# Optimization experiments

Measured on AMD Instinct MI355X. Metric: run time of the kernel, lower is better.

## Reference

```python
import jax, jax.numpy as jnp
import numpy as np

TWO_PI = 2.0 * np.pi
D_IN, N, P, C, BATCH = 784, 1024, 128, 10, 256
T, BETA, K_COUP, A_ANC = 0.5, 2.0, 1.0, 0.08
OMEGA_ANC = TWO_PI * 200.0
N_STEPS = 16  # fixed-grid RK4 steps over [0, T]


def setup_inputs() -> dict:
    key = jax.random.key(0)
    k0, k1, k2, k3 = jax.random.split(key, 4)
    x = jax.random.normal(k0, (BATCH, D_IN), dtype=jnp.float32)
    W_enc = jax.random.normal(k1, (N, D_IN), dtype=jnp.float32) * (1.0 / np.sqrt(D_IN))
    b_enc = jnp.zeros((N,), dtype=jnp.float32)
    xi = jax.random.uniform(k2, (P, N), dtype=jnp.float32) * TWO_PI  # memory patterns
    W_out = jax.random.normal(k3, (C, 2 * N), dtype=jnp.float32) * (1.0 / np.sqrt(2 * N))
    b_out = jnp.zeros((C,), dtype=jnp.float32)
    return {"x": x, "W_enc": W_enc, "b_enc": b_enc, "xi": xi, "W_out": W_out, "b_out": b_out}


def _dphi(t, phi, xi):
    # phi: (B, N), xi: (P, N) -> diff: (B, P, N)
    diff = phi[:, None, :] - xi[None, :, :]
    m = jnp.cos(diff).sum(-1)                               # (B, P) overlaps
    w = jax.nn.softmax(BETA * m / N, axis=-1)               # (B, P)
    coupling = jnp.einsum('bp,bpn->bn', w, jnp.sin(diff))   # (B, N)
    return K_COUP * coupling + A_ANC * jnp.sin(OMEGA_ANC * t - phi)


def reference(x, W_enc, b_enc, xi, W_out, b_out):
    # Encoder: phi0 in (0, 2pi)
    phi0 = TWO_PI * jax.nn.sigmoid(x @ W_enc.T + b_enc)
    dt = T / N_STEPS

    def step(phi, t):
        k1 = _dphi(t, phi, xi)
        k2 = _dphi(t + 0.5 * dt, phi + 0.5 * dt * k1, xi)
        k3 = _dphi(t + 0.5 * dt, phi + 0.5 * dt * k2, xi)
        k4 = _dphi(t + dt, phi + dt * k3, xi)
        return phi + (dt / 6.0) * (k1 + 2.0 * k2 + 2.0 * k3 + k4), None

    ts = jnp.arange(N_STEPS, dtype=jnp.float32) * dt
    phi_T, _ = jax.lax.scan(step, phi0, ts)
    # Readout on [cos, sin] features
    feats = jnp.concatenate([jnp.cos(phi_T), jnp.sin(phi_T)], axis=-1)
    return feats @ W_out.T + b_out
```

## Files before the change

### kernel.cpp

```cpp
#include <hip/hip_runtime.h>
#include <math.h>


typedef __attribute__((ext_vector_type(4))) float f32x4;
typedef __attribute__((ext_vector_type(2))) float f32x2;
typedef __attribute__((ext_vector_type(8))) short bf16x8;
typedef __attribute__((ext_vector_type(2))) unsigned short u16x2;
typedef __attribute__((ext_vector_type(2))) long i64x2;

struct TCons { float s[64]; float c[64]; };

__device__ __forceinline__ unsigned short f2bf(float f) {
  unsigned u = __builtin_bit_cast(unsigned, f);
  return (unsigned short)((u + 0x7FFFu + ((u >> 16) & 1u)) >> 16);
}
__device__ __forceinline__ long pk8fp8(const float* v) {
  unsigned lo = __builtin_amdgcn_cvt_pk_fp8_f32(v[0], v[1], 0, false);
  lo = __builtin_amdgcn_cvt_pk_fp8_f32(v[2], v[3], lo, true);
  unsigned hi = __builtin_amdgcn_cvt_pk_fp8_f32(v[4], v[5], 0, false);
  hi = __builtin_amdgcn_cvt_pk_fp8_f32(v[6], v[7], hi, true);
  return (long)lo | ((long)hi << 32);
}

#define A1_OFF    0
#define MBUF_OFF  8192
#define W_OFF     10304
#define ZP_OFF    10560
#define XST_OFF   10576
#define T2L_OFF   13904
#define RED_OFF   13904
#define LDS_BYTES 161360

__global__
__attribute__((amdgpu_flat_work_group_size(1024, 1024), amdgpu_waves_per_eu(4, 4)))
void phasenn_kernel(
    const float* __restrict__ x, const float* __restrict__ W_enc,
    const float* __restrict__ b_enc, const float* __restrict__ xi,
    const float* __restrict__ W_out, const float* __restrict__ b_out,
    float* __restrict__ dout, char* __restrict__ wsb, TCons tc)
{
  __shared__ __align__(16) char smem[LDS_BYTES];

  const int tid  = threadIdx.x;
  const int bk   = blockIdx.x;
  const int w    = tid >> 6;
  const int lane = tid & 63;
  const int q    = lane >> 4;
  const int b16  = lane & 15;
  const int row2 = b16 & 1;
  const int j4   = b16 >> 2;
  const int rp   = (b16 >> 1) & 1;
  const int swz  = row2 * 5;

  char* T1g = wsb;
  char* T2g = wsb + (256 << 10);

  if (tid < 4) *(unsigned*)(smem + ZP_OFF + tid*4) = 0;

  {
    const int row = tid >> 7, dg = tid & 127;
    if (row < 2 && dg < 100) {
      bf16x8 fr = {0,0,0,0,0,0,0,0};
      if (dg < 98) {
        f32x4 v0 = *(const f32x4*)(x + (bk*2 + row)*784 + dg*8);
        f32x4 v1 = *(const f32x4*)(x + (bk*2 + row)*784 + dg*8 + 4);
        #pragma unroll
        for (int i = 0; i < 8; ++i) fr[i] = (short)f2bf(i < 4 ? v0[i] : v1[i-4]);
      }
      *(bf16x8*)(smem + XST_OFF + row*1664 + (((dg ^ row) & 127) << 4)) = fr;
    }
  }

  if (w < 8) {
    const int p = w*16 + b16;
    for (int f = 0; f < 32; ++f) {
      const int n0 = f*32 + q*8;
      f32x4 v0 = *(const f32x4*)(xi + p*1024 + n0);
      f32x4 v1 = *(const f32x4*)(xi + p*1024 + n0 + 4);
      float cv[8], sv[8];
      #pragma unroll
      for (int i = 0; i < 8; ++i) {
        float xv = (i < 4) ? v0[i] : v1[i-4];
        sv[i] = __sinf(xv); cv[i] = __cosf(xv);
      }
      i64x2 pr; pr[0] = pk8fp8(cv); pr[1] = pk8fp8(sv);
      *(i64x2*)(T1g + (size_t)((w*32 + f)*64 + lane)*16) = pr;
    }
  } else {
    const int w2 = w - 8;
    for (int f = 0; f < 32; ++f) {
      const int ct = w2*8 + (f >> 2), pt2 = f & 3;
      const int n = ct*16 + b16;
      float cv[8], sv[8];
      #pragma unroll
      for (int i = 0; i < 8; ++i) {
        float xv = xi[(pt2*32 + q*8 + i)*1024 + n];
        sv[i] = __sinf(xv); cv[i] = __cosf(xv);
      }
      i64x2 pr; pr[0] = pk8fp8(cv); pr[1] = pk8fp8(sv);
      if (ct < 36)
        *(i64x2*)(smem + T2L_OFF + (size_t)((ct*4 + pt2)*64 + lane)*16) = pr;
      else
        *(i64x2*)(T2g + (size_t)((ct*4 + pt2)*64 + lane)*16) = pr;
    }
  }
  __syncthreads();

  float p0[2], ka[2], pwv[2];
  {
    f32x4 pac[4] = {{0,0,0,0},{0,0,0,0},{0,0,0,0},{0,0,0,0}};
    for (int kt = 0; kt < 25; ++kt) {
      const char* baddr =
          smem + XST_OFF + row2*1664 + ((((kt*4 + q) ^ row2) & 127) << 4);
      bf16x8 bfr = *(const bf16x8*)baddr;
      const int d = kt*32 + q*8;
      #pragma unroll
      for (int j = 0; j < 4; ++j) {
        bf16x8 afr = {0,0,0,0,0,0,0,0};
        if (d < 784) {
          const int n = (w*4 + j)*16 + b16;
          f32x4 v0 = *(const f32x4*)(W_enc + n*784 + d);
          f32x4 v1 = *(const f32x4*)(W_enc + n*784 + d + 4);
          #pragma unroll
          for (int i = 0; i < 8; ++i) afr[i] = (short)f2bf(i < 4 ? v0[i] : v1[i-4]);
        }
        pac[j] = __builtin_amdgcn_mfma_f32_16x16x32_bf16(afr, bfr, pac[j], 0, 0, 0);
      }
    }
    f32x4 pc = (j4==0) ? pac[0] : (j4==1) ? pac[1] : (j4==2) ? pac[2] : pac[3];
    float vA = rp ? pc[2] : pc[0];
    float vB = rp ? pc[3] : pc[1];
    const int n0 = (w*4 + j4)*16 + q*4 + rp*2;
    float ph0 = 6.283185307179586f / (1.0f + __expf(-(vA + b_enc[n0])));
    float ph1 = 6.283185307179586f / (1.0f + __expf(-(vB + b_enc[n0 + 1])));
    p0[0] = ph0; pwv[0] = ph0; ka[0] = 0.0f;
    p0[1] = ph1; pwv[1] = ph1; ka[1] = 0.0f;
  }

  const float dtf = 0.03125f, half = 0.015625f;
  const float sixth = (float)(0.03125/6.0);

  for (int e = 0; e < 64; ++e) {
    float csv[2], snv[2];
    {
      #pragma unroll
      for (int r = 0; r < 2; ++r) {
        snv[r] = __sinf(pwv[r]);
        csv[r] = __cosf(pwv[r]);
      }
      unsigned cp = __builtin_amdgcn_cvt_pk_fp8_f32(csv[0], csv[1], 0, false);
      unsigned sp = __builtin_amdgcn_cvt_pk_fp8_f32(snv[0], snv[1], 0, false);
      const int u = (w*4 + j4)*2 + (q >> 1);
      char* base = smem + A1_OFF + row2*2048 + ((q & 1) << 2) + rp*2;
      *(unsigned short*)(base + ((u ^ swz) << 3))        = (unsigned short)cp;
      *(unsigned short*)(base + 1024 + ((u ^ swz) << 3)) = (unsigned short)sp;
    }
    __syncthreads();

    {
      const int pt = w & 7, kh = w >> 3;
      f32x4 accC = {0.f, 0.f, 0.f, 0.f}, accS = {0.f, 0.f, 0.f, 0.f};
      const char* t1b = T1g + (size_t)((pt*32 + kh*16)*64 + lane)*16;
      const char* a1b = smem + A1_OFF + row2*2048;
      #pragma unroll 8
      for (int i2 = 0; i2 < 16; ++i2) {
        const int ktc = kh*16 + i2;
        i64x2 af = *(const i64x2*)(t1b + (size_t)i2*1024);
        long bc = *(const long*)(a1b + (((ktc*4 + q) ^ swz) << 3));
        long bs = *(const long*)(a1b + 1024 + (((ktc*4 + q) ^ swz) << 3));
        accC = __builtin_amdgcn_mfma_f32_16x16x32_fp8_fp8(af[0], bc, accC, 0, 0, 0);
        accS = __builtin_amdgcn_mfma_f32_16x16x32_fp8_fp8(af[1], bs, accS, 0, 0, 0);
      }
      if (b16 < 2) {
        f32x4 acc = accC + accS;
        *(f32x4*)(smem + MBUF_OFF + kh*1056 + b16*528 + ((pt*16 + q*4) << 2)) = acc;
      }
    }
    __syncthreads();

    if (w < 2) {
      const char* mb = smem + MBUF_OFF + w*528 + lane*8;
      f32x2 u0 = *(const f32x2*)(mb);
      f32x2 u1 = *(const f32x2*)(mb + 1056);
      float e0 = __expf((u0[0] + u1[0]) * 0.001953125f);
      float e1 = __expf((u0[1] + u1[1]) * 0.001953125f);
      float s = e0 + e1;
      #pragma unroll
      for (int off = 1; off < 64; off <<= 1) s += __shfl_xor(s, off, 64);
      const float inv64 = 64.0f / s;
      unsigned pk = __builtin_amdgcn_cvt_pk_fp8_f32(e0*inv64, e1*inv64, 0, false);
      const int pp = lane*2, u = pp >> 3;
      *(unsigned short*)(smem + W_OFF + w*128 + ((u ^ w) << 3) + (pp & 7)) =
          (unsigned short)pk;
    }
    __syncthreads();

    {
      const float swt = tc.s[e], cwt = tc.c[e];
      const int st = e & 3;
      long wfr[4];
      #pragma unroll
      for (int pt2 = 0; pt2 < 4; ++pt2)
        wfr[pt2] = *(const long*)(smem + W_OFF + row2*128 + (((pt2*4 + q) ^ row2) << 3));
      f32x4 aC[4] = {{0,0,0,0},{0,0,0,0},{0,0,0,0},{0,0,0,0}};
      f32x4 aS[4] = {{0,0,0,0},{0,0,0,0},{0,0,0,0},{0,0,0,0}};
      if (w < 9) {
        const char* t2Lb = smem + T2L_OFF + (size_t)(w*16*64 + lane)*16;
        #pragma unroll
        for (int c = 0; c < 4; ++c)
          #pragma unroll
          for (int pt2 = 0; pt2 < 4; ++pt2) {
            i64x2 tf = *(const i64x2*)(t2Lb + (size_t)(c*4 + pt2)*1024);
            aC[c] = __builtin_amdgcn_mfma_f32_16x16x32_fp8_fp8(tf[0], wfr[pt2], aC[c], 0,0,0);
            aS[c] = __builtin_amdgcn_mfma_f32_16x16x32_fp8_fp8(tf[1], wfr[pt2], aS[c], 0,0,0);
          }
      } else {
        const char* t2b = T2g + (size_t)(w*16*64 + lane)*16;
        #pragma unroll
        for (int c = 0; c < 4; ++c)
          #pragma unroll
          for (int pt2 = 0; pt2 < 4; ++pt2) {
            i64x2 tf = *(const i64x2*)(t2b + (size_t)(c*4 + pt2)*1024);
            aC[c] = __builtin_amdgcn_mfma_f32_16x16x32_fp8_fp8(tf[0], wfr[pt2], aC[c], 0,0,0);
            aS[c] = __builtin_amdgcn_mfma_f32_16x16x32_fp8_fp8(tf[1], wfr[pt2], aS[c], 0,0,0);
          }
      }
      f32x4 c4 = (j4==0) ? aC[0] : (j4==1) ? aC[1] : (j4==2) ? aC[2] : aC[3];
      f32x4 s4 = (j4==0) ? aS[0] : (j4==1) ? aS[1] : (j4==2) ? aS[2] : aS[3];
      float vC[2], vS[2];
      vC[0] = rp ? c4[2] : c4[0];  vC[1] = rp ? c4[3] : c4[1];
      vS[0] = rp ? s4[2] : s4[0];  vS[1] = rp ? s4[3] : s4[1];
      #pragma unroll
      for (int r = 0; r < 2; ++r) {
        float s_ = snv[r];
        float c_ = csv[r];
        float kv = (s_*vC[r] - c_*vS[r]) * 0.015625f
                 + 0.08f*(swt*c_ - cwt*s_);
        if (st == 0)      { ka[r]  = kv;           pwv[r] = p0[r] + kv*half; }
        else if (st == 1) { ka[r] += 2.0f*kv;      pwv[r] = p0[r] + kv*half; }
        else if (st == 2) { ka[r] += 2.0f*kv;      pwv[r] = p0[r] + kv*dtf;  }
        else { ka[r] += kv; p0[r] += ka[r]*sixth; pwv[r] = p0[r]; }
      }
    }
  }

  __syncthreads();
  {
    u16x2 cp, sp;
    #pragma unroll
    for (int r = 0; r < 2; ++r) {
      float ph = p0[r];
      cp[r] = f2bf(__cosf(ph)); sp[r] = f2bf(__sinf(ph));
    }
    const int cj = (w*4 + j4)*2 + (q >> 1);
    char* base = smem + A1_OFF + row2*4096 + ((q & 1) << 3) + rp*4;
    *(u16x2*)(base + ((cj ^ row2) << 4))        = cp;
    *(u16x2*)(base + ((cj ^ row2) << 4) + 2048) = sp;
  }
  __syncthreads();
  {
    f32x4 acc = {0.f, 0.f, 0.f, 0.f};
    #pragma unroll
    for (int i2 = 0; i2 < 4; ++i2) {
      const int kt = w*4 + i2;
      const int k = kt*32 + q*8;
      bf16x8 afr = {0,0,0,0,0,0,0,0};
      if (b16 < 10) {
        f32x4 v0 = *(const f32x4*)(W_out + b16*2048 + k);
        f32x4 v1 = *(const f32x4*)(W_out + b16*2048 + k + 4);
        #pragma unroll
        for (int i = 0; i < 8; ++i) afr[i] = (short)f2bf(i < 4 ? v0[i] : v1[i-4]);
      }
      const char* baddr = (b16 < 2)
          ? (smem + A1_OFF + b16*4096 + ((((kt*4 + q) ^ b16) & 255) << 4))
          : (smem + ZP_OFF);
      bf16x8 bfr = *(const bf16x8*)baddr;
      acc = __builtin_amdgcn_mfma_f32_16x16x32_bf16(afr, bfr, acc, 0, 0, 0);
    }
    *(f32x4*)(smem + RED_OFF + ((w*64 + lane) << 4)) = acc;
  }
  __syncthreads();
  if (tid < 64) {
    f32x4 s = {0.f, 0.f, 0.f, 0.f};
    #pragma unroll
    for (int w2 = 0; w2 < 16; ++w2)
      s += *(const f32x4*)(smem + RED_OFF + ((w2*64 + tid) << 4));
    const int b = tid & 15, q2 = tid >> 4;
    if (b < 2) {
      #pragma unroll
      for (int r = 0; r < 4; ++r) {
        const int cl = q2*4 + r;
        if (cl < 10)
          dout[(bk*2 + b)*10 + cl] = s[r] + b_out[cl];
      }
    }
  }
}

extern "C" void kernel_launch(void* const* d_in, const int* in_sizes, int n_in,
                              void* d_out, int out_size, void* d_ws, size_t ws_size,
                              hipStream_t stream) {
  (void)in_sizes; (void)n_in; (void)ws_size; (void)out_size;
  const float* x     = (const float*)d_in[0];
  const float* W_enc = (const float*)d_in[1];
  const float* b_enc = (const float*)d_in[2];
  const float* xi    = (const float*)d_in[3];
  const float* W_out = (const float*)d_in[4];
  const float* b_out = (const float*)d_in[5];
  float* out = (float*)d_out;
  char* wsb = (char*)d_ws;

  TCons tc;
  const double OME = 2.0 * 3.14159265358979323846 * 200.0;
  const double dtd = 0.03125;
  const double co[4] = {0.0, 0.5, 0.5, 1.0};
  for (int e = 0; e < 64; ++e) {
    double t = ((double)(e >> 2) + co[e & 3]) * dtd;
    tc.s[e] = (float)sin(OME * t);
    tc.c[e] = (float)cos(OME * t);
  }

  phasenn_kernel<<<dim3(128), dim3(1024), 0, stream>>>(
      x, W_enc, b_enc, xi, W_out, b_out, out, wsb, tc);
}
```

Measured before the change: 413.6 us.

## Switch phase-oscillator MFMA path from fp8 to int8 16x16x64

```diff
diff --git a/kernel.cpp b/kernel.cpp
--- a/kernel.cpp
+++ b/kernel.cpp
@@ -3,10 +3,9 @@
 
 
 typedef __attribute__((ext_vector_type(4))) float f32x4;
-typedef __attribute__((ext_vector_type(2))) float f32x2;
+typedef __attribute__((ext_vector_type(4))) int   i32x4;
 typedef __attribute__((ext_vector_type(8))) short bf16x8;
 typedef __attribute__((ext_vector_type(2))) unsigned short u16x2;
-typedef __attribute__((ext_vector_type(2))) long i64x2;
 
 struct TCons { float s[64]; float c[64]; };
 
@@ -14,12 +13,12 @@
   unsigned u = __builtin_bit_cast(unsigned, f);
   return (unsigned short)((u + 0x7FFFu + ((u >> 16) & 1u)) >> 16);
 }
-__device__ __forceinline__ long pk8fp8(const float* v) {
-  unsigned lo = __builtin_amdgcn_cvt_pk_fp8_f32(v[0], v[1], 0, false);
-  lo = __builtin_amdgcn_cvt_pk_fp8_f32(v[2], v[3], lo, true);
-  unsigned hi = __builtin_amdgcn_cvt_pk_fp8_f32(v[4], v[5], 0, false);
-  hi = __builtin_amdgcn_cvt_pk_fp8_f32(v[6], v[7], hi, true);
-  return (long)lo | ((long)hi << 32);
+__device__ __forceinline__ int pk4i8(const float* v) {
+  int a = __float2int_rn(v[0]*127.0f) & 255;
+  int b = __float2int_rn(v[1]*127.0f) & 255;
+  int c = __float2int_rn(v[2]*127.0f) & 255;
+  int d = __float2int_rn(v[3]*127.0f);
+  return a | (b << 8) | (c << 16) | (d << 24);
 }
 
 #define A1_OFF    0
@@ -50,7 +49,6 @@
   const int row2 = b16 & 1;
   const int j4   = b16 >> 2;
   const int rp   = (b16 >> 1) & 1;
-  const int swz  = row2 * 5;
 
   char* T1g = wsb;
   char* T2g = wsb + (256 << 10);
@@ -73,35 +71,40 @@
 
   if (w < 8) {
     const int p = w*16 + b16;
-    for (int f = 0; f < 32; ++f) {
-      const int n0 = f*32 + q*8;
+    for (int F = 0; F < 16; ++F) {
+      const int n0 = F*64 + q*16;
       f32x4 v0 = *(const f32x4*)(xi + p*1024 + n0);
       f32x4 v1 = *(const f32x4*)(xi + p*1024 + n0 + 4);
-      float cv[8], sv[8];
-      #pragma unroll
-      for (int i = 0; i < 8; ++i) {
-        float xv = (i < 4) ? v0[i] : v1[i-4];
+      f32x4 v2 = *(const f32x4*)(xi + p*1024 + n0 + 8);
+      f32x4 v3 = *(const f32x4*)(xi + p*1024 + n0 + 12);
+      float cv[16], sv[16];
+      #pragma unroll
+      for (int i = 0; i < 16; ++i) {
+        float xv = (i < 4) ? v0[i] : (i < 8) ? v1[i-4] : (i < 12) ? v2[i-8] : v3[i-12];
         sv[i] = __sinf(xv); cv[i] = __cosf(xv);
       }
-      i64x2 pr; pr[0] = pk8fp8(cv); pr[1] = pk8fp8(sv);
-      *(i64x2*)(T1g + (size_t)((w*32 + f)*64 + lane)*16) = pr;
+      i32x4 C = { pk4i8(cv), pk4i8(cv+4), pk4i8(cv+8), pk4i8(cv+12) };
+      i32x4 S = { pk4i8(sv), pk4i8(sv+4), pk4i8(sv+8), pk4i8(sv+12) };
+      char* dst = T1g + (size_t)(w*16 + F)*2048 + lane*32;
+      *(i32x4*)(dst) = C; *(i32x4*)(dst + 16) = S;
     }
   } else {
     const int w2 = w - 8;
-    for (int f = 0; f < 32; ++f) {
-      const int ct = w2*8 + (f >> 2), pt2 = f & 3;
+    for (int f = 0; f < 16; ++f) {
+      const int ct = w2*8 + (f >> 1), P2 = f & 1;
       const int n = ct*16 + b16;
-      float cv[8], sv[8];
-      #pragma unroll
-      for (int i = 0; i < 8; ++i) {
-        float xv = xi[(pt2*32 + q*8 + i)*1024 + n];
+      float cv[16], sv[16];
+      #pragma unroll
+      for (int i = 0; i < 16; ++i) {
+        float xv = xi[(P2*64 + q*16 + i)*1024 + n];
         sv[i] = __sinf(xv); cv[i] = __cosf(xv);
       }
-      i64x2 pr; pr[0] = pk8fp8(cv); pr[1] = pk8fp8(sv);
-      if (ct < 36)
-        *(i64x2*)(smem + T2L_OFF + (size_t)((ct*4 + pt2)*64 + lane)*16) = pr;
-      else
-        *(i64x2*)(T2g + (size_t)((ct*4 + pt2)*64 + lane)*16) = pr;
+      i32x4 C = { pk4i8(cv), pk4i8(cv+4), pk4i8(cv+8), pk4i8(cv+12) };
+      i32x4 S = { pk4i8(sv), pk4i8(sv+4), pk4i8(sv+8), pk4i8(sv+12) };
+      char* dst = (ct < 36)
+          ? (smem + T2L_OFF + (size_t)(ct*2 + P2)*2048 + lane*32)
+          : (T2g + (size_t)(ct*2 + P2)*2048 + lane*32);
+      *(i32x4*)(dst) = C; *(i32x4*)(dst + 16) = S;
     }
   }
   __syncthreads();
@@ -139,6 +142,8 @@
 
   const float dtf = 0.03125f, half = 0.015625f;
   const float sixth = (float)(0.03125/6.0);
+  const float mscale = (float)(2.0 / (1024.0 * 16129.0));
+  const float kscale = (float)(1.0 / 16129.0);
 
   for (int e = 0; e < 64; ++e) {
     float csv[2], snv[2];
@@ -148,93 +153,98 @@
         snv[r] = __sinf(pwv[r]);
         csv[r] = __cosf(pwv[r]);
       }
-      unsigned cp = __builtin_amdgcn_cvt_pk_fp8_f32(csv[0], csv[1], 0, false);
-      unsigned sp = __builtin_amdgcn_cvt_pk_fp8_f32(snv[0], snv[1], 0, false);
-      const int u = (w*4 + j4)*2 + (q >> 1);
-      char* base = smem + A1_OFF + row2*2048 + ((q & 1) << 2) + rp*2;
-      *(unsigned short*)(base + ((u ^ swz) << 3))        = (unsigned short)cp;
-      *(unsigned short*)(base + 1024 + ((u ^ swz) << 3)) = (unsigned short)sp;
+      int c0 = __float2int_rn(csv[0]*127.0f) & 255;
+      int c1 = __float2int_rn(csv[1]*127.0f) & 255;
+      int s0 = __float2int_rn(snv[0]*127.0f) & 255;
+      int s1 = __float2int_rn(snv[1]*127.0f) & 255;
+      const int n0 = (w*4 + j4)*16 + q*4 + rp*2;
+      char* base = smem + A1_OFF + row2*2048 + n0;
+      *(unsigned short*)(base)        = (unsigned short)(c0 | (c1 << 8));
+      *(unsigned short*)(base + 1024) = (unsigned short)(s0 | (s1 << 8));
     }
     __syncthreads();
 
     {
       const int pt = w & 7, kh = w >> 3;
-      f32x4 accC = {0.f, 0.f, 0.f, 0.f}, accS = {0.f, 0.f, 0.f, 0.f};
-      const char* t1b = T1g + (size_t)((pt*32 + kh*16)*64 + lane)*16;
+      i32x4 accC = {0,0,0,0}, accS = {0,0,0,0};
+      const char* t1b = T1g + (size_t)(pt*16 + kh*8)*2048 + lane*32;
       const char* a1b = smem + A1_OFF + row2*2048;
-      #pragma unroll 8
-      for (int i2 = 0; i2 < 16; ++i2) {
-        const int ktc = kh*16 + i2;
-        i64x2 af = *(const i64x2*)(t1b + (size_t)i2*1024);
-        long bc = *(const long*)(a1b + (((ktc*4 + q) ^ swz) << 3));
-        long bs = *(const long*)(a1b + 1024 + (((ktc*4 + q) ^ swz) << 3));
-        accC = __builtin_amdgcn_mfma_f32_16x16x32_fp8_fp8(af[0], bc, accC, 0, 0, 0);
-        accS = __builtin_amdgcn_mfma_f32_16x16x32_fp8_fp8(af[1], bs, accS, 0, 0, 0);
+      #pragma unroll
+      for (int i2 = 0; i2 < 8; ++i2) {
+        const int F = kh*8 + i2;
+        i32x4 ca = *(const i32x4*)(t1b + (size_t)i2*2048);
+        i32x4 sa = *(const i32x4*)(t1b + (size_t)i2*2048 + 16);
+        i32x4 bc = *(const i32x4*)(a1b + F*64 + q*16);
+        i32x4 bs = *(const i32x4*)(a1b + 1024 + F*64 + q*16);
+        accC = __builtin_amdgcn_mfma_i32_16x16x64_i8(ca, bc, accC, 0, 0, 0);
+        accS = __builtin_amdgcn_mfma_i32_16x16x64_i8(sa, bs, accS, 0, 0, 0);
       }
       if (b16 < 2) {
-        f32x4 acc = accC + accS;
-        *(f32x4*)(smem + MBUF_OFF + kh*1056 + b16*528 + ((pt*16 + q*4) << 2)) = acc;
+        i32x4 acc = accC + accS;
+        *(i32x4*)(smem + MBUF_OFF + kh*1056 + b16*528 + ((pt*16 + q*4) << 2)) = acc;
       }
     }
     __syncthreads();
 
     if (w < 2) {
       const char* mb = smem + MBUF_OFF + w*528 + lane*8;
-      f32x2 u0 = *(const f32x2*)(mb);
-      f32x2 u1 = *(const f32x2*)(mb + 1056);
-      float e0 = __expf((u0[0] + u1[0]) * 0.001953125f);
-      float e1 = __expf((u0[1] + u1[1]) * 0.001953125f);
+      int a0 = *(const int*)(mb),        a1 = *(const int*)(mb + 4);
+      int b0 = *(const int*)(mb + 1056), b1 = *(const int*)(mb + 1056 + 4);
+      float e0 = __expf((float)(a0 + b0) * mscale);
+      float e1 = __expf((float)(a1 + b1) * mscale);
       float s = e0 + e1;
       #pragma unroll
       for (int off = 1; off < 64; off <<= 1) s += __shfl_xor(s, off, 64);
-      const float inv64 = 64.0f / s;
-      unsigned pk = __builtin_amdgcn_cvt_pk_fp8_f32(e0*inv64, e1*inv64, 0, false);
-      const int pp = lane*2, u = pp >> 3;
-      *(unsigned short*)(smem + W_OFF + w*128 + ((u ^ w) << 3) + (pp & 7)) =
-          (unsigned short)pk;
+      const float inv = 127.0f / s;
+      int w0 = __float2int_rn(e0 * inv);
+      int w1 = __float2int_rn(e1 * inv);
+      *(unsigned short*)(smem + W_OFF + w*128 + lane*2) =
+          (unsigned short)((w0 & 255) | (w1 << 8));
     }
     __syncthreads();
 
     {
       const float swt = tc.s[e], cwt = tc.c[e];
       const int st = e & 3;
-      long wfr[4];
-      #pragma unroll
-      for (int pt2 = 0; pt2 < 4; ++pt2)
-        wfr[pt2] = *(const long*)(smem + W_OFF + row2*128 + (((pt2*4 + q) ^ row2) << 3));
-      f32x4 aC[4] = {{0,0,0,0},{0,0,0,0},{0,0,0,0},{0,0,0,0}};
-      f32x4 aS[4] = {{0,0,0,0},{0,0,0,0},{0,0,0,0},{0,0,0,0}};
+      i32x4 wf0 = *(const i32x4*)(smem + W_OFF + row2*128 + q*16);
+      i32x4 wf1 = *(const i32x4*)(smem + W_OFF + row2*128 + 64 + q*16);
+      i32x4 aC[4] = {{0,0,0,0},{0,0,0,0},{0,0,0,0},{0,0,0,0}};
+      i32x4 aS[4] = {{0,0,0,0},{0,0,0,0},{0,0,0,0},{0,0,0,0}};
       if (w < 9) {
-        const char* t2Lb = smem + T2L_OFF + (size_t)(w*16*64 + lane)*16;
+        const char* t2b = smem + T2L_OFF + (size_t)(w*8)*2048 + lane*32;
         #pragma unroll
         for (int c = 0; c < 4; ++c)
           #pragma unroll
-          for (int pt2 = 0; pt2 < 4; ++pt2) {
-            i64x2 tf = *(const i64x2*)(t2Lb + (size_t)(c*4 + pt2)*1024);
-            aC[c] = __builtin_amdgcn_mfma_f32_16x16x32_fp8_fp8(tf[0], wfr[pt2], aC[c], 0,0,0);
-            aS[c] = __builtin_amdgcn_mfma_f32_16x16x32_fp8_fp8(tf[1], wfr[pt2], aS[c], 0,0,0);
+          for (int P2 = 0; P2 < 2; ++P2) {
+            i32x4 ct_ = *(const i32x4*)(t2b + (size_t)(c*2 + P2)*2048);
+            i32x4 st_ = *(const i32x4*)(t2b + (size_t)(c*2 + P2)*2048 + 16);
+            i32x4 wf = P2 ? wf1 : wf0;
+            aC[c] = __builtin_amdgcn_mfma_i32_16x16x64_i8(ct_, wf, aC[c], 0, 0, 0);
+            aS[c] = __builtin_amdgcn_mfma_i32_16x16x64_i8(st_, wf, aS[c], 0, 0, 0);
           }
       } else {
-        const char* t2b = T2g + (size_t)(w*16*64 + lane)*16;
+        const char* t2b = T2g + (size_t)(w*8)*2048 + lane*32;
         #pragma unroll
         for (int c = 0; c < 4; ++c)
           #pragma unroll
-          for (int pt2 = 0; pt2 < 4; ++pt2) {
-            i64x2 tf = *(const i64x2*)(t2b + (size_t)(c*4 + pt2)*1024);
-            aC[c] = __builtin_amdgcn_mfma_f32_16x16x32_fp8_fp8(tf[0], wfr[pt2], aC[c], 0,0,0);
-            aS[c] = __builtin_amdgcn_mfma_f32_16x16x32_fp8_fp8(tf[1], wfr[pt2], aS[c], 0,0,0);
+          for (int P2 = 0; P2 < 2; ++P2) {
+            i32x4 ct_ = *(const i32x4*)(t2b + (size_t)(c*2 + P2)*2048);
+            i32x4 st_ = *(const i32x4*)(t2b + (size_t)(c*2 + P2)*2048 + 16);
+            i32x4 wf = P2 ? wf1 : wf0;
+            aC[c] = __builtin_amdgcn_mfma_i32_16x16x64_i8(ct_, wf, aC[c], 0, 0, 0);
+            aS[c] = __builtin_amdgcn_mfma_i32_16x16x64_i8(st_, wf, aS[c], 0, 0, 0);
           }
       }
-      f32x4 c4 = (j4==0) ? aC[0] : (j4==1) ? aC[1] : (j4==2) ? aC[2] : aC[3];
-      f32x4 s4 = (j4==0) ? aS[0] : (j4==1) ? aS[1] : (j4==2) ? aS[2] : aS[3];
+      i32x4 c4 = (j4==0) ? aC[0] : (j4==1) ? aC[1] : (j4==2) ? aC[2] : aC[3];
+      i32x4 s4 = (j4==0) ? aS[0] : (j4==1) ? aS[1] : (j4==2) ? aS[2] : aS[3];
       float vC[2], vS[2];
-      vC[0] = rp ? c4[2] : c4[0];  vC[1] = rp ? c4[3] : c4[1];
-      vS[0] = rp ? s4[2] : s4[0];  vS[1] = rp ? s4[3] : s4[1];
+      vC[0] = (float)(rp ? c4[2] : c4[0]);  vC[1] = (float)(rp ? c4[3] : c4[1]);
+      vS[0] = (float)(rp ? s4[2] : s4[0]);  vS[1] = (float)(rp ? s4[3] : s4[1]);
       #pragma unroll
       for (int r = 0; r < 2; ++r) {
         float s_ = snv[r];
         float c_ = csv[r];
-        float kv = (s_*vC[r] - c_*vS[r]) * 0.015625f
+        float kv = (s_*vC[r] - c_*vS[r]) * kscale
                  + 0.08f*(swt*c_ - cwt*s_);
         if (st == 0)      { ka[r]  = kv;           pwv[r] = p0[r] + kv*half; }
         else if (st == 1) { ka[r] += 2.0f*kv;      pwv[r] = p0[r] + kv*half; }
```

After: 451.1 us. 9.1% more time.
